# Optimization experiments

Hardware: AMD Instinct MI355X
Metric: run time of the kernel (lower is better)

The kernel has to match this reference:

```python
import jax, jax.numpy as jnp
import numpy as np

B, C, H, W = 4, 192, 56, 56


def setup_inputs() -> dict:
    key = jax.random.key(0)
    k1, k2, k3 = jax.random.split(key, 3)
    x = jax.random.normal(k1, (B, C, H, W), dtype=jnp.float32)
    conv_w = jax.random.normal(k2, (C, 2 * C), dtype=jnp.float32) * (1.0 / np.sqrt(2 * C))
    conv_b = jax.random.normal(k3, (C,), dtype=jnp.float32) * 0.01
    bn_gamma = jnp.ones((C,), dtype=jnp.float32)
    bn_beta = jnp.zeros((C,), dtype=jnp.float32)
    bn_mean = jnp.zeros((C,), dtype=jnp.float32)
    bn_var = jnp.ones((C,), dtype=jnp.float32)
    return {"x": x, "conv_w": conv_w, "conv_b": conv_b, "bn_gamma": bn_gamma,
            "bn_beta": bn_beta, "bn_mean": bn_mean, "bn_var": bn_var, "K": 4}


def reference(x, conv_w, conv_b, bn_gamma, bn_beta, bn_mean, bn_var, K):
    b, c, h, w = x.shape
    shifts_h = list(range(0, h, K))          # rolls along H
    shifts_w = list(range(K, w, K))          # rolls along W
    n = len(shifts_h) + len(shifts_w)
    scale = n ** (-0.5)
    # (B, n, C, H, W): all circularly shifted copies (static shift set)
    rolled = jnp.stack([jnp.roll(x, i, axis=2) for i in shifts_h] +
                       [jnp.roll(x, j, axis=3) for j in shifts_w], axis=1)
    # scores: tanh(scale * x * x_rolled), summed over channels -> (B, n, 1, H, W)
    scores = jnp.tanh(rolled * x[:, None] * scale).sum(axis=2, keepdims=True)
    weights = jax.nn.softmax(scores, axis=1)
    out = (rolled * weights).sum(axis=1)     # (B, C, H, W)
    cat = jnp.concatenate([x, out], axis=1)  # (B, 2C, H, W)
    # 1x1 conv as GEMM over channels
    y = jnp.einsum('bchw,oc->bohw', cat, conv_w) + conv_b[None, :, None, None]
    # BatchNorm2d in eval mode (running stats)
    eps = 1e-5
    inv = bn_gamma / jnp.sqrt(bn_var + eps)
    y = (y - bn_mean[None, :, None, None]) * inv[None, :, None, None] + bn_beta[None, :, None, None]
    return jax.nn.gelu(y, approximate=False)
```

## Files before the change

kernel.cpp:

```cpp
#include <hip/hip_runtime.h>
#include <hip/hip_bf16.h>
#include <hip/hip_fp16.h>
#include <math.h>

#define BB 4
#define CC 192
#define HH 56
#define WW 56
#define HWW 3136

typedef __attribute__((ext_vector_type(8))) short short8;
typedef __attribute__((ext_vector_type(4))) short short4v;
typedef __attribute__((ext_vector_type(8))) _Float16 half8;
typedef __attribute__((ext_vector_type(4))) float f32x4;

__device__ __forceinline__ unsigned short f2h(float f) {
    __half h = __float2half_rn(f);
    return __builtin_bit_cast(unsigned short, h);
}
__device__ __forceinline__ float2 h2f2(unsigned int u) {
    return __half22float2(__builtin_bit_cast(__half2, u));
}

__global__ __launch_bounds__(256) void k_pre(const float* __restrict__ x,
                                             const float* __restrict__ cw,
                                             unsigned short* __restrict__ xh16,
                                             unsigned short* __restrict__ wh16) {
    int tid = threadIdx.x, bid = blockIdx.x;
    if (bid < 2352) {
        __shared__ float tile[32][33];
        int b = bid / 588, rem = bid % 588;
        int by = rem / 98, bx = rem % 98;
        int tx = tid & 31, ty = tid >> 5;
        int p0 = bx * 32, c0 = by * 32;
#pragma unroll
        for (int i = 0; i < 4; i++) {
            int c = c0 + ty + 8 * i;
            tile[ty + 8 * i][tx] = x[(b * CC + c) * HWW + p0 + tx];
        }
        __syncthreads();
#pragma unroll
        for (int i = 0; i < 4; i++) {
            int p = p0 + ty + 8 * i;
            float v = tile[tx][ty + 8 * i];
            size_t o = (size_t)(b * HWW + p) * CC + c0 + tx;
            xh16[o] = f2h(v);
        }
    } else {
        int i = (bid - 2352) * 256 + tid;
        if (i < 384 * 192) {
            int n = i / 192, k = i % 192;
            float v = (n < 192) ? cw[n * 384 + k] : cw[(n - 192) * 384 + 192 + k];
            wh16[i] = f2h(v);
        }
    }
}

__global__ __launch_bounds__(256) void k_mid(const unsigned short* __restrict__ xh16,
                                             const unsigned short* __restrict__ wh16,
                                             float* __restrict__ sp,
                                             float* __restrict__ u,
                                             float* __restrict__ z) {
    __shared__ __align__(16) char smem[18432];
    int tid = threadIdx.x, bid = blockIdx.x;

    if (bid < 1792) {
        float* Xs = (float*)smem;
        const float K2L = 0.38490017945975050f * 1.4426950408889634f;
        bool isH = bid < 896;
        int lid = isH ? bid : bid - 896;
        int half = lid & 1;
        int rp = (lid >> 1) & 1;
        int cb2 = lid >> 2;
        int b = cb2 / 56, l0 = cb2 % 56;
        int r0 = rp * 2;

        const unsigned short* srcq = xh16 + (size_t)(b * HWW) * CC + half * 96;
        for (int idx = tid; idx < 28 * 12; idx += 256) {
            int t2 = idx / 12, cq = idx % 12;
            int pi = (r0 + t2 / 14) + 4 * (t2 % 14);
            int pix = isH ? (pi * WW + l0) : (l0 * WW + pi);
            uint4 hv = *(const uint4*)(srcq + (size_t)pix * CC + cq * 8);
            float2 f0 = h2f2(hv.x), f1 = h2f2(hv.y);
            float2 f2v = h2f2(hv.z), f3 = h2f2(hv.w);
            *(float4*)&Xs[t2 * 100 + cq * 8]     = make_float4(f0.x, f0.y, f1.x, f1.y);
            *(float4*)&Xs[t2 * 100 + cq * 8 + 4] = make_float4(f2v.x, f2v.y, f3.x, f3.y);
        }
        __syncthreads();

        int perCls = isH ? 105 : 91;
        if (tid < 2 * perCls) {
            int cls = tid / perCls, p = tid % perCls;
            int a, bb;
            if (isH) {
                a = (int)((sqrtf((float)(8 * p + 1)) - 1.0f) * 0.5f);
                bb = p - (a * (a + 1)) / 2;
            } else {
                int ap = (int)((sqrtf((float)(8 * p + 1)) - 1.0f) * 0.5f);
                bb = p - (ap * (ap + 1)) / 2;
                a = ap + 1;
            }
            const float* pA = &Xs[(cls * 14 + a) * 100];
            const float* pB = &Xs[(cls * 14 + bb) * 100];
            int lmod = (tid & 63) % 24;
            float s0 = 0.f, s1 = 0.f, s2 = 0.f, s3 = 0.f;
#pragma unroll
            for (int q = 0; q < 24; q++) {
                int qr = q + lmod; if (qr >= 24) qr -= 24;
                float4 av = *(const float4*)(pA + qr * 4);
                float4 bv = *(const float4*)(pB + qr * 4);
                s0 += __builtin_amdgcn_rcpf(__builtin_amdgcn_exp2f(av.x * bv.x * K2L) + 1.0f);
                s1 += __builtin_amdgcn_rcpf(__builtin_amdgcn_exp2f(av.y * bv.y * K2L) + 1.0f);
                s2 += __builtin_amdgcn_rcpf(__builtin_amdgcn_exp2f(av.z * bv.z * K2L) + 1.0f);
                s3 += __builtin_amdgcn_rcpf(__builtin_amdgcn_exp2f(av.w * bv.w * K2L) + 1.0f);
            }
            float s = 96.0f - 2.0f * (s0 + s1 + s2 + s3);
            int r = r0 + cls;
            size_t base = (size_t)(half * BB + b) * HWW;
            if (isH) {
                int i1 = a - bb;
                int h1 = r + 4 * a, h2 = r + 4 * bb;
                sp[(base + h1 * WW + l0) * 32 + i1] = s;
                if (a != bb) sp[(base + h2 * WW + l0) * 32 + (14 - i1)] = s;
            } else {
                int d = a - bb;
                int w1 = r + 4 * a, w2 = r + 4 * bb;
                sp[(base + l0 * WW + w1) * 32 + 14 + (d - 1)] = s;
                sp[(base + l0 * WW + w2) * 32 + 14 + (13 - d)] = s;
            }
        }
        return;
    }

    {
        unsigned short* Ah = (unsigned short*)smem;
        unsigned short* Bh = Ah + 64 * 72;
        float* Ds = (float*)smem;
        int vb = bid - 1792;
        int bm = (vb % 196) * 64, bn = (vb / 196) * 64;
        int lane = tid & 63, wv = tid >> 6;

        f32x4 acc[4] = {{0,0,0,0},{0,0,0,0},{0,0,0,0},{0,0,0,0}};

        for (int kc = 0; kc < 3; kc++) {
#pragma unroll
            for (int r2 = 0; r2 < 2; r2++) {
                int idx = tid + r2 * 256;
                int m = idx >> 3, kq = idx & 7;
                size_t ao = (size_t)(bm + m) * CC + kc * 64 + kq * 8;
                *(short8*)&Ah[m * 72 + kq * 8] = *(const short8*)(xh16 + ao);
                size_t bo = (size_t)(bn + m) * 192 + kc * 64 + kq * 8;
                *(short8*)&Bh[m * 72 + kq * 8] = *(const short8*)(wh16 + bo);
            }
            __syncthreads();
            int n0 = wv * 16;
            int k8 = lane >> 4;
            int col = lane & 15;
#pragma unroll
            for (int ks = 0; ks < 64; ks += 32) {
                int koff = ks + k8 * 8;
                half8 bf = *(const half8*)&Bh[(n0 + col) * 72 + koff];
#pragma unroll
                for (int fm = 0; fm < 4; fm++) {
                    half8 af = *(const half8*)&Ah[(fm * 16 + col) * 72 + koff];
                    acc[fm] = __builtin_amdgcn_mfma_f32_16x16x32_f16(af, bf, acc[fm], 0, 0, 0);
                }
            }
            __syncthreads();
        }
        {
            int col = lane & 15, rowq = lane >> 4;
#pragma unroll
            for (int fm = 0; fm < 4; fm++)
#pragma unroll
                for (int rg = 0; rg < 4; rg++)
                    Ds[(fm * 16 + rowq * 4 + rg) * 68 + wv * 16 + col] = acc[fm][rg];
        }
        __syncthreads();
        {
            int c4 = tid & 15, m0 = tid >> 4;
            int cg = bn + c4 * 4;
            float* dst = (cg < 192) ? u : z;
            int cc = (cg < 192) ? cg : cg - 192;
            int cc8 = cc >> 3, ci = cc & 7;
            size_t cbase = (size_t)cc8 * 100352;
#pragma unroll
            for (int p = 0; p < 4; p++) {
                int m = m0 + p * 16;
                int gp = bm + m;
                int b = gp / HWW, pp = gp - b * HWW;
                int hh = pp / 56, ww2 = pp - hh * 56;
                int rr = hh & 3, tt2 = hh >> 2;
                size_t off = cbase + ((size_t)((b * 4 + rr) * 14 + tt2)) * 448 + ww2 * 8 + ci;
                float4 v = *(float4*)&Ds[m * 68 + c4 * 4];
                *(float4*)&dst[off] = v;
            }
        }
    }
}

__global__ __launch_bounds__(448, 1) void k_tail(const float* __restrict__ u,
                                                 const float* __restrict__ z,
                                                 const float* __restrict__ sp,
                                                 const float* __restrict__ cb,
                                                 const float* __restrict__ gma,
                                                 const float* __restrict__ bta,
                                                 const float* __restrict__ mea,
                                                 const float* __restrict__ var,
                                                 float* __restrict__ y) {
    __shared__ __align__(16) char arena[25088 + 28224];
    float* Zs = (float*)arena;
    unsigned short* W16 = (unsigned short*)(arena + 25088);
    float* Ys = (float*)(arena + 25088);

    int tid = threadIdx.x, bid = blockIdx.x;
    int sl = bid & 31;
    int cc = bid >> 5;
    int th = sl & 1;
    int t2 = sl >> 1;
    int r = t2 & 3;
    int b = t2 >> 2;
    int w = tid >> 3, c = tid & 7;
    int cg = cc * 8 + c;
    int hbase = r + 4 * (th * 7);

    size_t slab = ((size_t)cc * BB + b) * 4 + r;
    const float* zg = z + slab * 6272;
    const float* ug = u + slab * 6272;

    float4 zva0 = *(const float4*)(zg + tid * 8);
    float4 zva1 = *(const float4*)(zg + tid * 8 + 4);
    float4 zvb0, zvb1;
    if (tid < 336) {
        zvb0 = *(const float4*)(zg + (tid + 448) * 8);
        zvb1 = *(const float4*)(zg + (tid + 448) * 8 + 4);
    }
    float acc0[7];
#pragma unroll
    for (int tt = 0; tt < 7; tt++)
        acc0[tt] = ug[(th * 7 + tt) * 448 + tid];

    if (tid < 392) {
        int tq = tid / 56, ww = tid - tq * 56;
        int row = hbase + 4 * tq;
        size_t gp = (size_t)b * HWW + row * WW + ww;
        const float4* p0 = (const float4*)&sp[gp * 32];
        const float4* p1 = (const float4*)&sp[((size_t)(4 * HWW) + gp) * 32];
        float sc[28];
#pragma unroll
        for (int j = 0; j < 7; j++) {
            float4 a4 = p0[j], v4 = p1[j];
            sc[4 * j + 0] = a4.x + v4.x; sc[4 * j + 1] = a4.y + v4.y;
            sc[4 * j + 2] = a4.z + v4.z; sc[4 * j + 3] = a4.w + v4.w;
        }
        float mx = -1e30f;
#pragma unroll
        for (int s = 0; s < 27; s++) mx = fmaxf(mx, sc[s]);
        float sum = 0.f;
#pragma unroll
        for (int s = 0; s < 27; s++) { sc[s] = __expf(sc[s] - mx); sum += sc[s]; }
        float inv = __builtin_amdgcn_rcpf(sum);
        unsigned short hw[28];
#pragma unroll
        for (int s = 0; s < 27; s++) hw[s] = f2h(sc[s] * inv);
        hw[27] = 0;
        unsigned short* d = &W16[tid * 36];
        *(short8*)(d)      = *(short8*)&hw[0];
        *(short8*)(d + 8)  = *(short8*)&hw[8];
        *(short8*)(d + 16) = *(short8*)&hw[16];
        *(short4v*)(d + 24) = *(short4v*)&hw[24];
    }

    {
        float* dst = &Zs[tid * 8];
        *(float4*)dst = zva0;
        *(float4*)(dst + 4) = zva1;
    }
    if (tid < 336) {
        float* dst = &Zs[(tid + 448) * 8];
        *(float4*)dst = zvb0;
        *(float4*)(dst + 4) = zvb1;
    }
    __syncthreads();

    float zc[14];
#pragma unroll
    for (int m = 0; m < 14; m++) {
        int t0 = m + th * 7;
        if (t0 >= 14) t0 -= 14;
        zc[m] = Zs[(t0 * 56 + w) * 8 + c];
    }

    float bias = cb[cg];
    float ginv = gma[cg] * rsqrtf(var[cg] + 1e-5f);
    float bt = bta[cg];
    float me = mea[cg];

    float vout[7];
#pragma unroll
    for (int tt = 0; tt < 7; tt++) {
        int t = th * 7 + tt;
        int pb = (tt * 56 + w) * 36;
        const uint2* wp = (const uint2*)&W16[pb];
        float a0 = acc0[tt], a1 = 0.f;
#pragma unroll
        for (int jj = 0; jj < 7; jj++) {
            uint2 rr2 = wp[jj];
            float2 fa = h2f2(rr2.x), fb = h2f2(rr2.y);
            float wv_[4] = {fa.x, fa.y, fb.x, fb.y};
#pragma unroll
            for (int e = 0; e < 4; e++) {
                int k = 4 * jj + e;
                if (k < 14) {
                    float zv = zc[(tt - k + 28) % 14];
                    if (e & 1) a1 += wv_[e] * zv; else a0 += wv_[e] * zv;
                } else if (k < 27) {
                    int j = k - 13;
                    int wj = w - 4 * j; if (wj < 0) wj += 56;
                    float zv = Zs[(t * 56 + wj) * 8 + c];
                    if (e & 1) a1 += wv_[e] * zv; else a0 += wv_[e] * zv;
                }
            }
        }
        float v = ((a0 + a1) + bias - me) * ginv + bt;
        vout[tt] = 0.5f * v * (1.0f + erff(v * 0.70710678118654752f));
    }

    __syncthreads();
#pragma unroll
    for (int tt = 0; tt < 7; tt++)
        Ys[tt * 448 + c * 56 + w] = vout[tt];
    __syncthreads();
    {
        int c_out = tid / 56, w_out = tid - c_out * 56;
        size_t ybase = ((size_t)(b * CC + cc * 8 + c_out)) * HWW + w_out;
#pragma unroll
        for (int tt = 0; tt < 7; tt++)
            y[ybase + (size_t)(hbase + 4 * tt) * 56] = Ys[tt * 448 + c_out * 56 + w_out];
    }
}

extern "C" void kernel_launch(void* const* d_in, const int* in_sizes, int n_in,
                              void* d_out, int out_size, void* d_ws, size_t ws_size,
                              hipStream_t stream) {
    const float* x   = (const float*)d_in[0];
    const float* cw  = (const float*)d_in[1];
    const float* cb  = (const float*)d_in[2];
    const float* gma = (const float*)d_in[3];
    const float* bta = (const float*)d_in[4];
    const float* mea = (const float*)d_in[5];
    const float* var = (const float*)d_in[6];
    float* out = (float*)d_out;

    float* ws = (float*)d_ws;
    float*          sp   = ws;
    float*          u    = ws + 802816;
    float*          z    = ws + 3211264;
    unsigned short* xh16 = (unsigned short*)(ws + 5619712);
    unsigned short* wh16 = (unsigned short*)(ws + 6823936);

    k_pre<<<2640, 256, 0, stream>>>(x, cw, xh16, wh16);
    k_mid<<<2968, 256, 0, stream>>>(xh16, wh16, sp, u, z);
    k_tail<<<768, 448, 0, stream>>>(u, z, sp, cb, gma, bta, mea, var, out);
}
```

Measured before the change: 119.0 us.

## Fuse fp16 pre-conversion into main kernel, reading fp32 input directly

Removes the separate pre-pass that transposed x to channel-last fp16 and converted the conv weights. The score blocks now gather fp32 values straight from NCHW x with strided scalar loads, and the GEMM blocks load fp32 x and weights and convert to fp16 while staging into shared memory. This saves a kernel launch and the round trip through the fp16 workspace, but the scoring loads become uncoalesced and each GEMM block repeats the weight conversion.

```diff
diff --git a/kernel.cpp b/kernel.cpp
--- a/kernel.cpp
+++ b/kernel.cpp
@@ -22,45 +22,11 @@
     return __half22float2(__builtin_bit_cast(__half2, u));
 }
 
-__global__ __launch_bounds__(256) void k_pre(const float* __restrict__ x,
-                                             const float* __restrict__ cw,
-                                             unsigned short* __restrict__ xh16,
-                                             unsigned short* __restrict__ wh16) {
-    int tid = threadIdx.x, bid = blockIdx.x;
-    if (bid < 2352) {
-        __shared__ float tile[32][33];
-        int b = bid / 588, rem = bid % 588;
-        int by = rem / 98, bx = rem % 98;
-        int tx = tid & 31, ty = tid >> 5;
-        int p0 = bx * 32, c0 = by * 32;
-#pragma unroll
-        for (int i = 0; i < 4; i++) {
-            int c = c0 + ty + 8 * i;
-            tile[ty + 8 * i][tx] = x[(b * CC + c) * HWW + p0 + tx];
-        }
-        __syncthreads();
-#pragma unroll
-        for (int i = 0; i < 4; i++) {
-            int p = p0 + ty + 8 * i;
-            float v = tile[tx][ty + 8 * i];
-            size_t o = (size_t)(b * HWW + p) * CC + c0 + tx;
-            xh16[o] = f2h(v);
-        }
-    } else {
-        int i = (bid - 2352) * 256 + tid;
-        if (i < 384 * 192) {
-            int n = i / 192, k = i % 192;
-            float v = (n < 192) ? cw[n * 384 + k] : cw[(n - 192) * 384 + 192 + k];
-            wh16[i] = f2h(v);
-        }
-    }
-}
-
-__global__ __launch_bounds__(256) void k_mid(const unsigned short* __restrict__ xh16,
-                                             const unsigned short* __restrict__ wh16,
-                                             float* __restrict__ sp,
-                                             float* __restrict__ u,
-                                             float* __restrict__ z) {
+__global__ __launch_bounds__(256) void k_main(const float* __restrict__ x,
+                                              const float* __restrict__ cw,
+                                              float* __restrict__ sp,
+                                              float* __restrict__ u,
+                                              float* __restrict__ z) {
     __shared__ __align__(16) char smem[18432];
     int tid = threadIdx.x, bid = blockIdx.x;
 
@@ -75,16 +41,12 @@
         int b = cb2 / 56, l0 = cb2 % 56;
         int r0 = rp * 2;
 
-        const unsigned short* srcq = xh16 + (size_t)(b * HWW) * CC + half * 96;
-        for (int idx = tid; idx < 28 * 12; idx += 256) {
-            int t2 = idx / 12, cq = idx % 12;
-            int pi = (r0 + t2 / 14) + 4 * (t2 % 14);
+        const float* srcx = x + ((size_t)(b * CC) + half * 96) * HWW;
+        for (int i = tid; i < 96 * 28; i += 256) {
+            int ch = i / 28, t2 = i - ch * 28;
+            int pi = (r0 + (t2 / 14)) + 4 * (t2 % 14);
             int pix = isH ? (pi * WW + l0) : (l0 * WW + pi);
-            uint4 hv = *(const uint4*)(srcq + (size_t)pix * CC + cq * 8);
-            float2 f0 = h2f2(hv.x), f1 = h2f2(hv.y);
-            float2 f2v = h2f2(hv.z), f3 = h2f2(hv.w);
-            *(float4*)&Xs[t2 * 100 + cq * 8]     = make_float4(f0.x, f0.y, f1.x, f1.y);
-            *(float4*)&Xs[t2 * 100 + cq * 8 + 4] = make_float4(f2v.x, f2v.y, f3.x, f3.y);
+            Xs[t2 * 100 + ch] = srcx[(size_t)ch * HWW + pix];
         }
         __syncthreads();
 
@@ -140,17 +102,50 @@
         int bm = (vb % 196) * 64, bn = (vb / 196) * 64;
         int lane = tid & 63, wv = tid >> 6;
 
+        int bb_ = bm / HWW;
+        int pl = bm - bb_ * HWW;
+        const float* xA = x + (size_t)(bb_ * CC) * HWW + pl;
+        bool isU = (bn < 192);
+
+        int ch2 = tid >> 3;
+        int mg = (tid & 7) * 8;
+        int kg = mg;
+
         f32x4 acc[4] = {{0,0,0,0},{0,0,0,0},{0,0,0,0},{0,0,0,0}};
 
         for (int kc = 0; kc < 3; kc++) {
-#pragma unroll
-            for (int r2 = 0; r2 < 2; r2++) {
-                int idx = tid + r2 * 256;
-                int m = idx >> 3, kq = idx & 7;
-                size_t ao = (size_t)(bm + m) * CC + kc * 64 + kq * 8;
-                *(short8*)&Ah[m * 72 + kq * 8] = *(const short8*)(xh16 + ao);
-                size_t bo = (size_t)(bn + m) * 192 + kc * 64 + kq * 8;
-                *(short8*)&Bh[m * 72 + kq * 8] = *(const short8*)(wh16 + bo);
+            {
+                int ca = kc * 64 + 2 * ch2;
+                const float* s0 = xA + (size_t)ca * HWW + mg;
+                const float* s1 = s0 + HWW;
+                float4 a0 = *(const float4*)s0;
+                float4 a1 = *(const float4*)(s0 + 4);
+                float4 b0 = *(const float4*)s1;
+                float4 b1 = *(const float4*)(s1 + 4);
+                float av[8] = {a0.x, a0.y, a0.z, a0.w, a1.x, a1.y, a1.z, a1.w};
+                float bv[8] = {b0.x, b0.y, b0.z, b0.w, b1.x, b1.y, b1.z, b1.w};
+#pragma unroll
+                for (int j = 0; j < 8; j++) {
+                    unsigned int pk = (unsigned int)f2h(av[j]) |
+                                      ((unsigned int)f2h(bv[j]) << 16);
+                    *(unsigned int*)&Ah[(mg + j) * 72 + 2 * ch2] = pk;
+                }
+            }
+            {
+                int rr0 = bn + 2 * ch2;
+                const float* w0 = isU ? (cw + (size_t)rr0 * 384 + kc * 64 + kg)
+                                      : (cw + (size_t)(rr0 - 192) * 384 + 192 + kc * 64 + kg);
+                const float* w1 = w0 + 384;
+                float4 c0 = *(const float4*)w0;
+                float4 c1 = *(const float4*)(w0 + 4);
+                float4 d0 = *(const float4*)w1;
+                float4 d1 = *(const float4*)(w1 + 4);
+                unsigned short h0[8] = {f2h(c0.x), f2h(c0.y), f2h(c0.z), f2h(c0.w),
+                                        f2h(c1.x), f2h(c1.y), f2h(c1.z), f2h(c1.w)};
+                unsigned short h1[8] = {f2h(d0.x), f2h(d0.y), f2h(d0.z), f2h(d0.w),
+                                        f2h(d1.x), f2h(d1.y), f2h(d1.z), f2h(d1.w)};
+                *(short8*)&Bh[(2 * ch2) * 72 + kg]     = *(short8*)h0;
+                *(short8*)&Bh[(2 * ch2 + 1) * 72 + kg] = *(short8*)h1;
             }
             __syncthreads();
             int n0 = wv * 16;
@@ -353,13 +348,10 @@
     float* out = (float*)d_out;
 
     float* ws = (float*)d_ws;
-    float*          sp   = ws;
-    float*          u    = ws + 802816;
-    float*          z    = ws + 3211264;
-    unsigned short* xh16 = (unsigned short*)(ws + 5619712);
-    unsigned short* wh16 = (unsigned short*)(ws + 6823936);
-
-    k_pre<<<2640, 256, 0, stream>>>(x, cw, xh16, wh16);
-    k_mid<<<2968, 256, 0, stream>>>(xh16, wh16, sp, u, z);
+    float* sp = ws;
+    float* u  = ws + 802816;
+    float* z  = ws + 3211264;
+
+    k_main<<<2968, 256, 0, stream>>>(x, cw, sp, u, z);
     k_tail<<<768, 448, 0, stream>>>(u, z, sp, cb, gma, bta, mea, var, out);
 }
```

New measurement: 126.0 us. +5.9%, slower.
